# Kernel tuning notes

Hardware: AMD Instinct MI355X
Metric: run time of the kernel (lower is better)

The kernel has to match this reference:

```python
import jax, jax.numpy as jnp
import numpy as np

N_NODES = 100000
N_EDGES = 3200000
NCLASSES = 4
IN_DIM = 2          # per-node feature dim -> edge in_feats = 2*IN_DIM = 4
HID = 8             # output_dim


def setup_inputs() -> dict:
    key = jax.random.key(0)
    k_m, k_e, k_w1, k_b1, k_w2, k_b2 = jax.random.split(key, 6)
    m = jax.random.normal(k_m, (N_NODES, NCLASSES, IN_DIM), dtype=jnp.float32)
    edge_index = jax.random.randint(k_e, (2, N_EDGES), 0, N_NODES, dtype=jnp.int64)
    in_feats = 2 * IN_DIM
    # ClasswiseLinear: one independent Linear per class (grouped weights)
    s1 = 1.0 / np.sqrt(in_feats)
    s2 = 1.0 / np.sqrt(HID)
    W1 = jax.random.uniform(k_w1, (NCLASSES, in_feats, HID), jnp.float32, -s1, s1)
    b1 = jax.random.uniform(k_b1, (NCLASSES, HID), jnp.float32, -s1, s1)
    W2 = jax.random.uniform(k_w2, (NCLASSES, HID, 1), jnp.float32, -s2, s2)
    b2 = jax.random.uniform(k_b2, (NCLASSES, 1), jnp.float32, -s2, s2)
    return {"m": m, "edge_index": edge_index, "W1": W1, "b1": b1, "W2": W2, "b2": b2}


def reference(m, edge_index, W1, b1, W2, b2):
    row, col = edge_index[0], edge_index[1]
    # gather node features per edge; concat dest/src -> [E, C, 2*IN_DIM]
    B = jnp.concatenate([m[col], m[row]], axis=-1)
    B = jax.lax.stop_gradient(B)  # original code calls .detach()
    # classwise linear 1 + tanh: grouped GEMM over class axis c
    h = jnp.tanh(jnp.einsum("eci,cih->ech", B, W1) + b1)      # [E, C, HID]
    o = jnp.tanh(jnp.einsum("ech,cho->eco", h, W2) + b2)      # [E, C, 1]
    # softmax over the class dimension (dim=1)
    return jax.nn.softmax(o, axis=1)
```

## Files before the change

### kernel.cpp

```cpp
#include <hip/hip_runtime.h>

#define TWO_LOG2E 2.8853901817779268f
#define LOG2E     1.4426950408889634f

template<int CTRL>
__device__ __forceinline__ float dpp_qperm(float x) {
    int r = __builtin_amdgcn_update_dpp(0, __float_as_int(x), CTRL, 0xF, 0xF, true);
    return __int_as_float(r);
}

__device__ __forceinline__ float tanh_pre(float hs) {
    float e = __builtin_amdgcn_exp2f(hs);
    float r = __builtin_amdgcn_rcpf(e + 1.0f);
    return fmaf(-2.0f, r, 1.0f);
}

__global__ __launch_bounds__(256, 4) void edge_mlp(
    const float* __restrict__ m,
    const int*   __restrict__ eidx,
    const float* __restrict__ W1,
    const float* __restrict__ b1,
    const float* __restrict__ W2,
    const float* __restrict__ b2,
    float*       __restrict__ out,
    const int nE)
{
    const int tid0 = blockIdx.x * blockDim.x + threadIdx.x;
    const int c = tid0 & 3;
    const int cc2 = c * 2;

    float w1[32];
    #pragma unroll
    for (int k = 0; k < 8; ++k) {
        float4 v = *(const float4*)(W1 + c*32 + 4*k);
        w1[4*k+0] = v.x * TWO_LOG2E; w1[4*k+1] = v.y * TWO_LOG2E;
        w1[4*k+2] = v.z * TWO_LOG2E; w1[4*k+3] = v.w * TWO_LOG2E;
    }
    float bb1[8];
    #pragma unroll
    for (int j = 0; j < 8; ++j) bb1[j] = b1[c*8 + j] * TWO_LOG2E;
    float w2[8];
    #pragma unroll
    for (int j = 0; j < 8; ++j) w2[j] = W2[c*8 + j] * TWO_LOG2E;
    float b2s = b2[c] * TWO_LOG2E;

    #pragma unroll
    for (int i = 0; i < 32; ++i) asm volatile("" : "+v"(w1[i]));
    #pragma unroll
    for (int j = 0; j < 8; ++j)  asm volatile("" : "+v"(bb1[j]));
    #pragma unroll
    for (int j = 0; j < 8; ++j)  asm volatile("" : "+v"(w2[j]));
    asm volatile("" : "+v"(b2s));

    const int* eidx1 = eidx + nE;
    const int total  = nE * 4;
    const int stride = gridDim.x * blockDim.x;

    constexpr int UN = 4;
    int t = tid0;

    for (; t + (UN - 1) * stride < total; t += UN * stride) {
        int row[UN], col[UN];
        #pragma unroll
        for (int k = 0; k < UN; ++k) {
            const int e = (t + k * stride) >> 2;
            row[k] = __builtin_nontemporal_load(eidx + e);
            col[k] = __builtin_nontemporal_load(eidx1 + e);
        }
        float2 mc[UN], mr[UN];
        #pragma unroll
        for (int k = 0; k < UN; ++k) {
            mc[k] = *(const float2*)(m + (unsigned)col[k] * 8u + cc2);
            mr[k] = *(const float2*)(m + (unsigned)row[k] * 8u + cc2);
        }
        #pragma unroll
        for (int k = 0; k < UN; ++k) {
            float o = b2s;
            #pragma unroll
            for (int j = 0; j < 8; ++j) {
                float h = bb1[j];
                h = fmaf(mc[k].x, w1[j],      h);
                h = fmaf(mc[k].y, w1[8 + j],  h);
                h = fmaf(mr[k].x, w1[16 + j], h);
                h = fmaf(mr[k].y, w1[24 + j], h);
                o = fmaf(tanh_pre(h), w2[j], o);
            }
            const float to = tanh_pre(o);
            const float eo = __builtin_amdgcn_exp2f(to * LOG2E);
            float s = eo + dpp_qperm<0xB1>(eo);
            s = s + dpp_qperm<0x4E>(s);
            __builtin_nontemporal_store(eo * __builtin_amdgcn_rcpf(s),
                                        out + (t + k * stride));
        }
    }

    for (; t < total; t += stride) {
        const int e = t >> 2;
        const int r0 = eidx[e];
        const int c0 = eidx1[e];
        const float2 mcv = *(const float2*)(m + (unsigned)c0 * 8u + cc2);
        const float2 mrv = *(const float2*)(m + (unsigned)r0 * 8u + cc2);
        float o = b2s;
        #pragma unroll
        for (int j = 0; j < 8; ++j) {
            float h = bb1[j];
            h = fmaf(mcv.x, w1[j],      h);
            h = fmaf(mcv.y, w1[8 + j],  h);
            h = fmaf(mrv.x, w1[16 + j], h);
            h = fmaf(mrv.y, w1[24 + j], h);
            o = fmaf(tanh_pre(h), w2[j], o);
        }
        const float to = tanh_pre(o);
        const float eo = __builtin_amdgcn_exp2f(to * LOG2E);
        float s = eo + dpp_qperm<0xB1>(eo);
        s = s + dpp_qperm<0x4E>(s);
        out[t] = eo * __builtin_amdgcn_rcpf(s);
    }
}

extern "C" void kernel_launch(void* const* d_in, const int* in_sizes, int n_in,
                              void* d_out, int out_size, void* d_ws, size_t ws_size,
                              hipStream_t stream) {
    const float* m  = (const float*)d_in[0];
    const int* eidx = (const int*)d_in[1];
    const float* W1 = (const float*)d_in[2];
    const float* b1 = (const float*)d_in[3];
    const float* W2 = (const float*)d_in[4];
    const float* b2 = (const float*)d_in[5];
    float* out = (float*)d_out;
    const int nE = in_sizes[1] / 2;

    const int threads = 256;
    const int blocks  = 2048;
    hipLaunchKernelGGL(edge_mlp, dim3(blocks), dim3(threads), 0, stream,
                       m, eidx, W1, b1, W2, b2, out, nE);
}
```

Before: 60.59 us.

## Software-pipeline edge index and feature gathers across loop iterations

Restructures the main loop so the edge indices for the next group are prefetched before computing the current group, and the node-feature gathers for the next group are issued after the current compute. This is meant to hide gather latency behind the tanh/MLP arithmetic. It also folds the final tanh and the log2e scaling into a single exp2 fma, removes the asm register-pinning barriers, raises the occupancy hint to 5 waves per SIMD, and changes the grid from 2048 to 1250 blocks. The extra live registers for the prefetched data may pressure the tighter register budget.

Result: slower. 63.51 us (+4.8%).

```diff
diff --git a/kernel.cpp b/kernel.cpp
--- a/kernel.cpp
+++ b/kernel.cpp
@@ -15,7 +15,7 @@
     return fmaf(-2.0f, r, 1.0f);
 }
 
-__global__ __launch_bounds__(256, 4) void edge_mlp(
+__global__ __launch_bounds__(256, 5) void edge_mlp(
     const float* __restrict__ m,
     const int*   __restrict__ eidx,
     const float* __restrict__ W1,
@@ -42,36 +42,44 @@
     float w2[8];
     #pragma unroll
     for (int j = 0; j < 8; ++j) w2[j] = W2[c*8 + j] * TWO_LOG2E;
-    float b2s = b2[c] * TWO_LOG2E;
-
-    #pragma unroll
-    for (int i = 0; i < 32; ++i) asm volatile("" : "+v"(w1[i]));
-    #pragma unroll
-    for (int j = 0; j < 8; ++j)  asm volatile("" : "+v"(bb1[j]));
-    #pragma unroll
-    for (int j = 0; j < 8; ++j)  asm volatile("" : "+v"(w2[j]));
-    asm volatile("" : "+v"(b2s));
+    const float b2s = b2[c] * TWO_LOG2E;
 
     const int* eidx1 = eidx + nE;
     const int total  = nE * 4;
     const int stride = gridDim.x * blockDim.x;
+    constexpr int UN = 4;
+    const int step = UN * stride;
 
-    constexpr int UN = 4;
     int t = tid0;
+    int   row[UN], col[UN];
+    float2 mc[UN], mr[UN];
 
-    for (; t + (UN - 1) * stride < total; t += UN * stride) {
-        int row[UN], col[UN];
+    bool have = (t + (UN - 1) * stride < total);
+    if (have) {
         #pragma unroll
         for (int k = 0; k < UN; ++k) {
             const int e = (t + k * stride) >> 2;
             row[k] = __builtin_nontemporal_load(eidx + e);
             col[k] = __builtin_nontemporal_load(eidx1 + e);
         }
-        float2 mc[UN], mr[UN];
         #pragma unroll
         for (int k = 0; k < UN; ++k) {
             mc[k] = *(const float2*)(m + (unsigned)col[k] * 8u + cc2);
             mr[k] = *(const float2*)(m + (unsigned)row[k] * 8u + cc2);
+        }
+    }
+
+    while (have) {
+        const int tn = t + step;
+        const bool haveN = (tn + (UN - 1) * stride < total);
+        int rowN[UN], colN[UN];
+        if (haveN) {
+            #pragma unroll
+            for (int k = 0; k < UN; ++k) {
+                const int e = (tn + k * stride) >> 2;
+                rowN[k] = __builtin_nontemporal_load(eidx + e);
+                colN[k] = __builtin_nontemporal_load(eidx1 + e);
+            }
         }
         #pragma unroll
         for (int k = 0; k < UN; ++k) {
@@ -85,17 +93,27 @@
                 h = fmaf(mr[k].y, w1[24 + j], h);
                 o = fmaf(tanh_pre(h), w2[j], o);
             }
-            const float to = tanh_pre(o);
-            const float eo = __builtin_amdgcn_exp2f(to * LOG2E);
+            const float e2 = __builtin_amdgcn_exp2f(o);
+            const float r2 = __builtin_amdgcn_rcpf(e2 + 1.0f);
+            const float eo = __builtin_amdgcn_exp2f(fmaf(-TWO_LOG2E, r2, LOG2E));
             float s = eo + dpp_qperm<0xB1>(eo);
             s = s + dpp_qperm<0x4E>(s);
             __builtin_nontemporal_store(eo * __builtin_amdgcn_rcpf(s),
                                         out + (t + k * stride));
         }
+        if (haveN) {
+            #pragma unroll
+            for (int k = 0; k < UN; ++k) {
+                mc[k] = *(const float2*)(m + (unsigned)colN[k] * 8u + cc2);
+                mr[k] = *(const float2*)(m + (unsigned)rowN[k] * 8u + cc2);
+            }
+        }
+        t = tn;
+        have = haveN;
     }
 
     for (; t < total; t += stride) {
-        const int e = t >> 2;
+        const int e  = t >> 2;
         const int r0 = eidx[e];
         const int c0 = eidx1[e];
         const float2 mcv = *(const float2*)(m + (unsigned)c0 * 8u + cc2);
@@ -110,8 +128,9 @@
             h = fmaf(mrv.y, w1[24 + j], h);
             o = fmaf(tanh_pre(h), w2[j], o);
         }
-        const float to = tanh_pre(o);
-        const float eo = __builtin_amdgcn_exp2f(to * LOG2E);
+        const float e2 = __builtin_amdgcn_exp2f(o);
+        const float r2 = __builtin_amdgcn_rcpf(e2 + 1.0f);
+        const float eo = __builtin_amdgcn_exp2f(fmaf(-TWO_LOG2E, r2, LOG2E));
         float s = eo + dpp_qperm<0xB1>(eo);
         s = s + dpp_qperm<0x4E>(s);
         out[t] = eo * __builtin_amdgcn_rcpf(s);
@@ -131,7 +150,7 @@
     const int nE = in_sizes[1] / 2;
 
     const int threads = 256;
-    const int blocks  = 2048;
+    const int blocks  = 1250;
     hipLaunchKernelGGL(edge_mlp, dim3(blocks), dim3(threads), 0, stream,
                        m, eidx, W1, b1, W2, b2, out, nE);
 }
```

## Replace grid-stride loop with one-shot blocks of 512 outputs per 128 threads

Applied to the files above, without the earlier changes.

Changes the launch from a fixed 2048-block grid-stride persistent kernel to a non-persistent grid where each 128-thread block covers 512 outputs, each thread handling 4 outputs spaced 64 apart. Edge-index loads are issued before the weight loads so the dependent gather latency overlaps the weight setup, and the final tanh is folded into the softmax exponent with a single fma. This removes loop overhead and the register-pinning asm, but adds per-block weight reload cost and many more blocks (25000).

After: 82.20 us. 1.36x slower.

```diff
diff --git a/kernel.cpp b/kernel.cpp
--- a/kernel.cpp
+++ b/kernel.cpp
@@ -9,13 +9,7 @@
     return __int_as_float(r);
 }
 
-__device__ __forceinline__ float tanh_pre(float hs) {
-    float e = __builtin_amdgcn_exp2f(hs);
-    float r = __builtin_amdgcn_rcpf(e + 1.0f);
-    return fmaf(-2.0f, r, 1.0f);
-}
-
-__global__ __launch_bounds__(256, 4) void edge_mlp(
+__global__ __launch_bounds__(128) void edge_mlp(
     const float* __restrict__ m,
     const int*   __restrict__ eidx,
     const float* __restrict__ W1,
@@ -25,56 +19,45 @@
     float*       __restrict__ out,
     const int nE)
 {
-    const int tid0 = blockIdx.x * blockDim.x + threadIdx.x;
-    const int c = tid0 & 3;
+    const int total = nE * 4;
+    const int t0 = blockIdx.x * 512 + ((threadIdx.x >> 6) << 8) + (threadIdx.x & 63);
+    const int c  = threadIdx.x & 3;
     const int cc2 = c * 2;
+    const int e0 = t0 >> 2;
+    const int* eidx1 = eidx + nE;
 
-    float w1[32];
-    #pragma unroll
-    for (int k = 0; k < 8; ++k) {
-        float4 v = *(const float4*)(W1 + c*32 + 4*k);
-        w1[4*k+0] = v.x * TWO_LOG2E; w1[4*k+1] = v.y * TWO_LOG2E;
-        w1[4*k+2] = v.z * TWO_LOG2E; w1[4*k+3] = v.w * TWO_LOG2E;
-    }
-    float bb1[8];
-    #pragma unroll
-    for (int j = 0; j < 8; ++j) bb1[j] = b1[c*8 + j] * TWO_LOG2E;
-    float w2[8];
-    #pragma unroll
-    for (int j = 0; j < 8; ++j) w2[j] = W2[c*8 + j] * TWO_LOG2E;
-    float b2s = b2[c] * TWO_LOG2E;
+    if (t0 + 192 < total) {
+        int row[4], col[4];
+        #pragma unroll
+        for (int k = 0; k < 4; ++k) {
+            row[k] = __builtin_nontemporal_load(eidx  + e0 + 16 * k);
+            col[k] = __builtin_nontemporal_load(eidx1 + e0 + 16 * k);
+        }
 
-    #pragma unroll
-    for (int i = 0; i < 32; ++i) asm volatile("" : "+v"(w1[i]));
-    #pragma unroll
-    for (int j = 0; j < 8; ++j)  asm volatile("" : "+v"(bb1[j]));
-    #pragma unroll
-    for (int j = 0; j < 8; ++j)  asm volatile("" : "+v"(w2[j]));
-    asm volatile("" : "+v"(b2s));
+        float w1[32];
+        #pragma unroll
+        for (int k = 0; k < 8; ++k) {
+            float4 v = *(const float4*)(W1 + c * 32 + 4 * k);
+            w1[4*k+0] = v.x * TWO_LOG2E; w1[4*k+1] = v.y * TWO_LOG2E;
+            w1[4*k+2] = v.z * TWO_LOG2E; w1[4*k+3] = v.w * TWO_LOG2E;
+        }
+        float bb1[8];
+        #pragma unroll
+        for (int j = 0; j < 8; ++j) bb1[j] = b1[c*8 + j] * TWO_LOG2E;
+        float w2[8];
+        #pragma unroll
+        for (int j = 0; j < 8; ++j) w2[j] = W2[c*8 + j] * TWO_LOG2E;
+        const float b2s = b2[c] * TWO_LOG2E;
 
-    const int* eidx1 = eidx + nE;
-    const int total  = nE * 4;
-    const int stride = gridDim.x * blockDim.x;
-
-    constexpr int UN = 4;
-    int t = tid0;
-
-    for (; t + (UN - 1) * stride < total; t += UN * stride) {
-        int row[UN], col[UN];
+        float2 mc[4], mr[4];
         #pragma unroll
-        for (int k = 0; k < UN; ++k) {
-            const int e = (t + k * stride) >> 2;
-            row[k] = __builtin_nontemporal_load(eidx + e);
-            col[k] = __builtin_nontemporal_load(eidx1 + e);
-        }
-        float2 mc[UN], mr[UN];
-        #pragma unroll
-        for (int k = 0; k < UN; ++k) {
+        for (int k = 0; k < 4; ++k) {
             mc[k] = *(const float2*)(m + (unsigned)col[k] * 8u + cc2);
             mr[k] = *(const float2*)(m + (unsigned)row[k] * 8u + cc2);
         }
+
         #pragma unroll
-        for (int k = 0; k < UN; ++k) {
+        for (int k = 0; k < 4; ++k) {
             float o = b2s;
             #pragma unroll
             for (int j = 0; j < 8; ++j) {
@@ -83,38 +66,62 @@
                 h = fmaf(mc[k].y, w1[8 + j],  h);
                 h = fmaf(mr[k].x, w1[16 + j], h);
                 h = fmaf(mr[k].y, w1[24 + j], h);
-                o = fmaf(tanh_pre(h), w2[j], o);
+                const float e = __builtin_amdgcn_exp2f(h);
+                const float r = __builtin_amdgcn_rcpf(e + 1.0f);
+                o = fmaf(fmaf(-2.0f, r, 1.0f), w2[j], o);
             }
-            const float to = tanh_pre(o);
-            const float eo = __builtin_amdgcn_exp2f(to * LOG2E);
+            const float e2 = __builtin_amdgcn_exp2f(o);
+            const float r2 = __builtin_amdgcn_rcpf(e2 + 1.0f);
+            const float eo = __builtin_amdgcn_exp2f(fmaf(-TWO_LOG2E, r2, LOG2E));
             float s = eo + dpp_qperm<0xB1>(eo);
             s = s + dpp_qperm<0x4E>(s);
             __builtin_nontemporal_store(eo * __builtin_amdgcn_rcpf(s),
-                                        out + (t + k * stride));
+                                        out + t0 + 64 * k);
         }
-    }
+    } else {
+        float w1[32];
+        #pragma unroll
+        for (int k = 0; k < 8; ++k) {
+            float4 v = *(const float4*)(W1 + c * 32 + 4 * k);
+            w1[4*k+0] = v.x * TWO_LOG2E; w1[4*k+1] = v.y * TWO_LOG2E;
+            w1[4*k+2] = v.z * TWO_LOG2E; w1[4*k+3] = v.w * TWO_LOG2E;
+        }
+        float bb1[8];
+        #pragma unroll
+        for (int j = 0; j < 8; ++j) bb1[j] = b1[c*8 + j] * TWO_LOG2E;
+        float w2[8];
+        #pragma unroll
+        for (int j = 0; j < 8; ++j) w2[j] = W2[c*8 + j] * TWO_LOG2E;
+        const float b2s = b2[c] * TWO_LOG2E;
 
-    for (; t < total; t += stride) {
-        const int e = t >> 2;
-        const int r0 = eidx[e];
-        const int c0 = eidx1[e];
-        const float2 mcv = *(const float2*)(m + (unsigned)c0 * 8u + cc2);
-        const float2 mrv = *(const float2*)(m + (unsigned)r0 * 8u + cc2);
-        float o = b2s;
         #pragma unroll
-        for (int j = 0; j < 8; ++j) {
-            float h = bb1[j];
-            h = fmaf(mcv.x, w1[j],      h);
-            h = fmaf(mcv.y, w1[8 + j],  h);
-            h = fmaf(mrv.x, w1[16 + j], h);
-            h = fmaf(mrv.y, w1[24 + j], h);
-            o = fmaf(tanh_pre(h), w2[j], o);
+        for (int k = 0; k < 4; ++k) {
+            const int t = t0 + 64 * k;
+            if (t >= total) break;
+            const int e  = t >> 2;
+            const int r0 = eidx[e];
+            const int c0 = eidx1[e];
+            const float2 mcv = *(const float2*)(m + (unsigned)c0 * 8u + cc2);
+            const float2 mrv = *(const float2*)(m + (unsigned)r0 * 8u + cc2);
+            float o = b2s;
+            #pragma unroll
+            for (int j = 0; j < 8; ++j) {
+                float h = bb1[j];
+                h = fmaf(mcv.x, w1[j],      h);
+                h = fmaf(mcv.y, w1[8 + j],  h);
+                h = fmaf(mrv.x, w1[16 + j], h);
+                h = fmaf(mrv.y, w1[24 + j], h);
+                const float e1 = __builtin_amdgcn_exp2f(h);
+                const float r1 = __builtin_amdgcn_rcpf(e1 + 1.0f);
+                o = fmaf(fmaf(-2.0f, r1, 1.0f), w2[j], o);
+            }
+            const float e2 = __builtin_amdgcn_exp2f(o);
+            const float r2 = __builtin_amdgcn_rcpf(e2 + 1.0f);
+            const float eo = __builtin_amdgcn_exp2f(fmaf(-TWO_LOG2E, r2, LOG2E));
+            float s = eo + dpp_qperm<0xB1>(eo);
+            s = s + dpp_qperm<0x4E>(s);
+            out[t] = eo * __builtin_amdgcn_rcpf(s);
         }
-        const float to = tanh_pre(o);
-        const float eo = __builtin_amdgcn_exp2f(to * LOG2E);
-        float s = eo + dpp_qperm<0xB1>(eo);
-        s = s + dpp_qperm<0x4E>(s);
-        out[t] = eo * __builtin_amdgcn_rcpf(s);
     }
 }
 
@@ -130,8 +137,8 @@
     float* out = (float*)d_out;
     const int nE = in_sizes[1] / 2;
 
-    const int threads = 256;
-    const int blocks  = 2048;
-    hipLaunchKernelGGL(edge_mlp, dim3(blocks), dim3(threads), 0, stream,
+    const int total  = nE * 4;
+    const int blocks = (total + 511) / 512;
+    hipLaunchKernelGGL(edge_mlp, dim3(blocks), dim3(128), 0, stream,
                        m, eidx, W1, b1, W2, b2, out, nE);
 }
```

## Pair reciprocals in hidden tanh, fold constants, polynomial exp, deeper unroll

Applied to the files above, without the earlier changes.

Rewrites the hidden-layer tanh so that two units share one reciprocal: rcp(a0*a1) multiplied by the other factor. The constant part of 1-2r is folded into the output bias via the W2 sum. The final softmax exp is replaced by a degree-6 polynomial in y, which is valid because tanh keeps y in [-1,1]. It also raises the unroll from 4 to 8 edges, removes the occupancy hint, and drops the asm register pinning, all aimed at cutting transcendental-unit pressure and hiding more gather latency, at the cost of register pressure and a small accuracy change.

New measurement: 67.82 us. +11.9%, slower.

```diff
diff --git a/kernel.cpp b/kernel.cpp
--- a/kernel.cpp
+++ b/kernel.cpp
@@ -2,6 +2,8 @@
 
 #define TWO_LOG2E 2.8853901817779268f
 #define LOG2E     1.4426950408889634f
+
+typedef float f32x2 __attribute__((ext_vector_type(2)));
 
 template<int CTRL>
 __device__ __forceinline__ float dpp_qperm(float x) {
@@ -9,13 +11,7 @@
     return __int_as_float(r);
 }
 
-__device__ __forceinline__ float tanh_pre(float hs) {
-    float e = __builtin_amdgcn_exp2f(hs);
-    float r = __builtin_amdgcn_rcpf(e + 1.0f);
-    return fmaf(-2.0f, r, 1.0f);
-}
-
-__global__ __launch_bounds__(256, 4) void edge_mlp(
+__global__ __launch_bounds__(256) void edge_mlp(
     const float* __restrict__ m,
     const int*   __restrict__ eidx,
     const float* __restrict__ W1,
@@ -39,24 +35,21 @@
     float bb1[8];
     #pragma unroll
     for (int j = 0; j < 8; ++j) bb1[j] = b1[c*8 + j] * TWO_LOG2E;
-    float w2[8];
+    float w2n[8];
+    float w2sum = 0.0f;
     #pragma unroll
-    for (int j = 0; j < 8; ++j) w2[j] = W2[c*8 + j] * TWO_LOG2E;
-    float b2s = b2[c] * TWO_LOG2E;
-
-    #pragma unroll
-    for (int i = 0; i < 32; ++i) asm volatile("" : "+v"(w1[i]));
-    #pragma unroll
-    for (int j = 0; j < 8; ++j)  asm volatile("" : "+v"(bb1[j]));
-    #pragma unroll
-    for (int j = 0; j < 8; ++j)  asm volatile("" : "+v"(w2[j]));
-    asm volatile("" : "+v"(b2s));
+    for (int j = 0; j < 8; ++j) {
+        const float w = W2[c*8 + j];
+        w2n[j] = -2.0f * TWO_LOG2E * w;
+        w2sum += w;
+    }
+    const float o0 = TWO_LOG2E * (b2[c] + w2sum);
 
     const int* eidx1 = eidx + nE;
     const int total  = nE * 4;
     const int stride = gridDim.x * blockDim.x;
 
-    constexpr int UN = 4;
+    constexpr int UN = 8;
     int t = tid0;
 
     for (; t + (UN - 1) * stride < total; t += UN * stride) {
@@ -64,57 +57,79 @@
         #pragma unroll
         for (int k = 0; k < UN; ++k) {
             const int e = (t + k * stride) >> 2;
-            row[k] = __builtin_nontemporal_load(eidx + e);
+            row[k] = __builtin_nontemporal_load(eidx  + e);
             col[k] = __builtin_nontemporal_load(eidx1 + e);
         }
-        float2 mc[UN], mr[UN];
+        f32x2 mc[UN], mr[UN];
         #pragma unroll
         for (int k = 0; k < UN; ++k) {
-            mc[k] = *(const float2*)(m + (unsigned)col[k] * 8u + cc2);
-            mr[k] = *(const float2*)(m + (unsigned)row[k] * 8u + cc2);
+            mc[k] = *(const f32x2*)(m + (unsigned)col[k] * 8u + cc2);
+            mr[k] = *(const f32x2*)(m + (unsigned)row[k] * 8u + cc2);
         }
         #pragma unroll
         for (int k = 0; k < UN; ++k) {
-            float o = b2s;
+            float o = o0;
             #pragma unroll
-            for (int j = 0; j < 8; ++j) {
-                float h = bb1[j];
-                h = fmaf(mc[k].x, w1[j],      h);
-                h = fmaf(mc[k].y, w1[8 + j],  h);
-                h = fmaf(mr[k].x, w1[16 + j], h);
-                h = fmaf(mr[k].y, w1[24 + j], h);
-                o = fmaf(tanh_pre(h), w2[j], o);
+            for (int j = 0; j < 8; j += 2) {
+                float h0 = bb1[j], h1 = bb1[j+1];
+                h0 = fmaf(mc[k].x, w1[j],      h0); h1 = fmaf(mc[k].x, w1[j+1],    h1);
+                h0 = fmaf(mc[k].y, w1[8 + j],  h0); h1 = fmaf(mc[k].y, w1[9 + j],  h1);
+                h0 = fmaf(mr[k].x, w1[16 + j], h0); h1 = fmaf(mr[k].x, w1[17 + j], h1);
+                h0 = fmaf(mr[k].y, w1[24 + j], h0); h1 = fmaf(mr[k].y, w1[25 + j], h1);
+                const float a0 = __builtin_amdgcn_exp2f(h0) + 1.0f;
+                const float a1 = __builtin_amdgcn_exp2f(h1) + 1.0f;
+                const float inv = __builtin_amdgcn_rcpf(a0 * a1);
+                o = fmaf(w2n[j],   inv * a1, o);
+                o = fmaf(w2n[j+1], inv * a0, o);
             }
-            const float to = tanh_pre(o);
-            const float eo = __builtin_amdgcn_exp2f(to * LOG2E);
-            float s = eo + dpp_qperm<0xB1>(eo);
+            const float e2 = __builtin_amdgcn_exp2f(o);
+            const float r2 = __builtin_amdgcn_rcpf(e2 + 1.0f);
+            const float y  = fmaf(-2.0f, r2, 1.0f);
+            float p = fmaf(y, 0.0013888889f, 0.0083333333f);
+            p = fmaf(p, y, 0.0416666667f);
+            p = fmaf(p, y, 0.1666666667f);
+            p = fmaf(p, y, 0.5f);
+            p = fmaf(p, y, 1.0f);
+            p = fmaf(p, y, 1.0f);
+            float s = p + dpp_qperm<0xB1>(p);
             s = s + dpp_qperm<0x4E>(s);
-            __builtin_nontemporal_store(eo * __builtin_amdgcn_rcpf(s),
+            __builtin_nontemporal_store(p * __builtin_amdgcn_rcpf(s),
                                         out + (t + k * stride));
         }
     }
 
     for (; t < total; t += stride) {
-        const int e = t >> 2;
+        const int e  = t >> 2;
         const int r0 = eidx[e];
         const int c0 = eidx1[e];
-        const float2 mcv = *(const float2*)(m + (unsigned)c0 * 8u + cc2);
-        const float2 mrv = *(const float2*)(m + (unsigned)r0 * 8u + cc2);
-        float o = b2s;
+        const f32x2 mcv = *(const f32x2*)(m + (unsigned)c0 * 8u + cc2);
+        const f32x2 mrv = *(const f32x2*)(m + (unsigned)r0 * 8u + cc2);
+        float o = o0;
         #pragma unroll
-        for (int j = 0; j < 8; ++j) {
-            float h = bb1[j];
-            h = fmaf(mcv.x, w1[j],      h);
-            h = fmaf(mcv.y, w1[8 + j],  h);
-            h = fmaf(mrv.x, w1[16 + j], h);
-            h = fmaf(mrv.y, w1[24 + j], h);
-            o = fmaf(tanh_pre(h), w2[j], o);
+        for (int j = 0; j < 8; j += 2) {
+            float h0 = bb1[j], h1 = bb1[j+1];
+            h0 = fmaf(mcv.x, w1[j],      h0); h1 = fmaf(mcv.x, w1[j+1],    h1);
+            h0 = fmaf(mcv.y, w1[8 + j],  h0); h1 = fmaf(mcv.y, w1[9 + j],  h1);
+            h0 = fmaf(mrv.x, w1[16 + j], h0); h1 = fmaf(mrv.x, w1[17 + j], h1);
+            h0 = fmaf(mrv.y, w1[24 + j], h0); h1 = fmaf(mrv.y, w1[25 + j], h1);
+            const float a0 = __builtin_amdgcn_exp2f(h0) + 1.0f;
+            const float a1 = __builtin_amdgcn_exp2f(h1) + 1.0f;
+            const float inv = __builtin_amdgcn_rcpf(a0 * a1);
+            o = fmaf(w2n[j],   inv * a1, o);
+            o = fmaf(w2n[j+1], inv * a0, o);
         }
-        const float to = tanh_pre(o);
-        const float eo = __builtin_amdgcn_exp2f(to * LOG2E);
-        float s = eo + dpp_qperm<0xB1>(eo);
+        const float e2 = __builtin_amdgcn_exp2f(o);
+        const float r2 = __builtin_amdgcn_rcpf(e2 + 1.0f);
+        const float y  = fmaf(-2.0f, r2, 1.0f);
+        float p = fmaf(y, 0.0013888889f, 0.0083333333f);
+        p = fmaf(p, y, 0.0416666667f);
+        p = fmaf(p, y, 0.1666666667f);
+        p = fmaf(p, y, 0.5f);
+        p = fmaf(p, y, 1.0f);
+        p = fmaf(p, y, 1.0f);
+        float s = p + dpp_qperm<0xB1>(p);
         s = s + dpp_qperm<0x4E>(s);
-        out[t] = eo * __builtin_amdgcn_rcpf(s);
+        out[t] = p * __builtin_amdgcn_rcpf(s);
     }
 }
 
```
